# Kernel tuning notes

Measured on AMD Instinct MI355X. Metric: run time of the kernel, lower is better.

## Reference

```python
import jax, jax.numpy as jnp
import numpy as np

K = 10          # number of clusters (static; matches randint fill_max)
ALPHA = 0.02    # intra-cluster margin
DELTA = 0.5     # inter-cluster margin
LAMBDA_INTRA = 1.0
LAMBDA_INTER = 1.0
MIN_WEIGHT = 50.0


def setup_inputs() -> dict:
    key = jax.random.key(0)
    k1, k2 = jax.random.split(key)
    x = jax.random.normal(k1, (8, 64, 240, 320), dtype=jnp.float32)
    # module assumes NORMALIZED unit vectors along channel dim
    x = x / jnp.maximum(jnp.linalg.norm(x, axis=1, keepdims=True), 1e-12)
    cluster_masks = jax.random.randint(k2, (8, 1, 240, 320), 0, K, dtype=jnp.int32)
    return {"x": x, "cluster_masks": cluster_masks}


def reference(x, cluster_masks):
    B, C, H, W = x.shape
    cm = cluster_masks[:, 0]  # (B, H, W) int
    # one-hot cluster assignment; out-of-range ids (e.g. -1 = unlabeled) -> all zeros
    onehot = jax.nn.one_hot(cm, K, dtype=x.dtype)  # (B, H, W, K)

    # ---- spherical cluster means (fused segment-reduce over H*W) ----
    sums = jnp.einsum('bchw,bhwk->bck', x, onehot)          # (B, C, K)
    counts = jnp.sum(onehot, axis=(1, 2))                    # (B, K)
    means = sums / (counts[:, None, :] + 1e-10)
    # F.normalize(p=2, dim=1): x / max(||x||, eps)
    means = means / jnp.maximum(jnp.linalg.norm(means, axis=1, keepdims=True), 1e-12)

    # ---- broadcast means back to pixels ----
    tiled = jnp.einsum('bck,bhwk->bchw', means, onehot)      # (B, C, H, W)

    labeled = (cm >= 0).astype(x.dtype)                      # (B, H, W)
    # cosine metric
    intra_d = labeled * (0.5 * (1.0 - jnp.sum(x * tiled, axis=1)))  # (B, H, W)

    # ---- per-cluster hard-example weighting ----
    indicator = (intra_d > ALPHA).astype(x.dtype)            # (B, H, W)
    N_k = jnp.einsum('bhw,bhwk->bk', indicator, onehot)      # (B, K)
    weights = jnp.einsum('bk,bhwk->bhw', N_k, onehot)        # (B, H, W)
    weights = jnp.maximum(weights, MIN_WEIGHT) * K
    intra_loss = jnp.sum(intra_d ** 2 / weights) / B
    intra_loss = LAMBDA_INTRA * jnp.where(jnp.sum(indicator) > 0, intra_loss, 0.0)

    # ---- inter-cluster hinge loss (K > 1 statically) ----
    inter_d = 0.5 * (1.0 - jnp.einsum('bck,bcl->bkl', means, means))  # (B, K, K)
    hinge = jnp.maximum(DELTA - inter_d, 0.0) * (1.0 - jnp.eye(K, dtype=x.dtype))
    inter_loss = LAMBDA_INTER * jnp.sum(hinge ** 2) / (K * (K - 1) / 2 * B)

    loss = intra_loss + inter_loss
    return (loss, intra_loss, inter_loss)
```

## Files before the change

kernel.cpp:

```cpp
#include <hip/hip_runtime.h>

#define B_ 8
#define C_ 64
#define H_ 240
#define W_ 320
#define HW_ (H_ * W_)
#define HW4_ (HW_ / 4)
#define K_ 10
#define ALPHA_ 0.02f
#define DELTA_ 0.5f
#define MIN_WEIGHT_ 50.0f

#define NCH 4
#define CB_ (C_ / NCH)
#define Z1 8
#define CHUNK1 (HW4_ / Z1)

#define OFF_SUMS 0
#define OFF_CNT  5120
#define OFF_S2   5200
#define OFF_NK   5280
#define OFF_MEANS 5360

__global__ __launch_bounds__(256) void k1_sums(
    const float* __restrict__ x, const int* __restrict__ cm,
    float* __restrict__ ws) {
  const int cb = blockIdx.x;
  const int b = blockIdx.y;
  const int z = blockIdx.z;
  const int tid = threadIdx.x;
  const int c0 = cb * NCH;

  const int lo = z * CHUNK1;
  const int hi = lo + CHUNK1;

  float* __restrict__ sums = ws + OFF_SUMS;
  float* __restrict__ counts = ws + OFF_CNT;

  const float4* __restrict__ xp =
      (const float4*)(x + (size_t)(b * C_ + c0) * HW_);
  const int4* __restrict__ cp = (const int4*)(cm + (size_t)b * HW_);

  float acc[NCH][K_];
#pragma unroll
  for (int c = 0; c < NCH; ++c)
#pragma unroll
    for (int j = 0; j < K_; ++j) acc[c][j] = 0.f;
  float cnt[K_];
#pragma unroll
  for (int j = 0; j < K_; ++j) cnt[j] = 0.f;
  const bool do_cnt = (cb == 0);

  for (int i = lo + tid; i < hi; i += 256) {
    const int4 k4 = cp[i];
    float oh0[K_], oh1[K_], oh2[K_], oh3[K_];
#pragma unroll
    for (int j = 0; j < K_; ++j) {
      oh0[j] = (k4.x == j) ? 1.f : 0.f;
      oh1[j] = (k4.y == j) ? 1.f : 0.f;
      oh2[j] = (k4.z == j) ? 1.f : 0.f;
      oh3[j] = (k4.w == j) ? 1.f : 0.f;
    }
    if (do_cnt) {
#pragma unroll
      for (int j = 0; j < K_; ++j)
        cnt[j] += (oh0[j] + oh1[j]) + (oh2[j] + oh3[j]);
    }
#pragma unroll
    for (int c = 0; c < NCH; ++c) {
      const float4 v = xp[c * HW4_ + i];
#pragma unroll
      for (int j = 0; j < K_; ++j) {
        acc[c][j] += v.x * oh0[j];
        acc[c][j] += v.y * oh1[j];
        acc[c][j] += v.z * oh2[j];
        acc[c][j] += v.w * oh3[j];
      }
    }
  }

#pragma unroll
  for (int c = 0; c < NCH; ++c) {
#pragma unroll
    for (int j = 0; j < K_; ++j) {
      float v = acc[c][j];
#pragma unroll
      for (int off = 32; off > 0; off >>= 1) v += __shfl_down(v, off, 64);
      if ((tid & 63) == 0)
        atomicAdd(&sums[(b * C_ + c0 + c) * K_ + j], v);
    }
  }
  if (do_cnt) {
#pragma unroll
    for (int j = 0; j < K_; ++j) {
      float v = cnt[j];
#pragma unroll
      for (int off = 32; off > 0; off >>= 1) v += __shfl_down(v, off, 64);
      if ((tid & 63) == 0) atomicAdd(&counts[b * K_ + j], v);
    }
  }
}

__global__ __launch_bounds__(256) void k2_norm(float* __restrict__ ws) {
  const int b = blockIdx.x;
  const int tid = threadIdx.x;

  const float* __restrict__ sums = ws + OFF_SUMS + b * C_ * K_;
  const float* __restrict__ counts = ws + OFF_CNT + b * K_;
  float* __restrict__ means = ws + OFF_MEANS + b * C_ * K_;

  __shared__ float mlds[C_ * K_];
  __shared__ float nrm[K_];

  for (int i = tid; i < C_ * K_; i += 256)
    mlds[i] = sums[i] / (counts[i % K_] + 1e-10f);
  __syncthreads();
  if (tid < K_) {
    float n2 = 0.f;
#pragma unroll
    for (int c = 0; c < C_; ++c) {
      const float mm = mlds[c * K_ + tid];
      n2 += mm * mm;
    }
    nrm[tid] = 1.f / fmaxf(sqrtf(n2), 1e-12f);
  }
  __syncthreads();
  for (int i = tid; i < C_ * K_; i += 256)
    means[i] = mlds[i] * nrm[i % K_];
}

__global__ __launch_bounds__(128) void k3_intra(
    const float* __restrict__ x, const int* __restrict__ cm,
    float* __restrict__ ws) {
  const int b = blockIdx.y;
  const int tid = threadIdx.x;
  const int w = tid >> 6;

  float* __restrict__ S2 = ws + OFF_S2;
  float* __restrict__ Nk = ws + OFF_NK;
  const float* __restrict__ means = ws + OFF_MEANS;

  __shared__ float mlds[C_ * K_];
  __shared__ float s2w[2 * K_];
  __shared__ float nkw[2 * K_];

  for (int i = tid; i < C_ * K_; i += 128) mlds[i] = means[b * C_ * K_ + i];
  if (tid < 2 * K_) { s2w[tid] = 0.f; nkw[tid] = 0.f; }
  __syncthreads();

  const int p4 = blockIdx.x * 128 + tid;
  const int4 k4 = ((const int4*)(cm + (size_t)b * HW_))[p4];
  const float4* __restrict__ xb =
      (const float4*)(x + (size_t)b * C_ * HW_) + p4;

  const float* __restrict__ m0 = &mlds[k4.x];
  const float* __restrict__ m1 = &mlds[k4.y];
  const float* __restrict__ m2 = &mlds[k4.z];
  const float* __restrict__ m3 = &mlds[k4.w];

  float d0 = 0.f, d1 = 0.f, d2 = 0.f, d3 = 0.f;
#pragma unroll 16
  for (int c = 0; c < C_; ++c) {
    const float4 v = xb[c * HW4_];
    d0 += v.x * m0[c * K_];
    d1 += v.y * m1[c * K_];
    d2 += v.z * m2[c * K_];
    d3 += v.w * m3[c * K_];
  }

  const float i0 = 0.5f * (1.f - d0);
  const float i1 = 0.5f * (1.f - d1);
  const float i2 = 0.5f * (1.f - d2);
  const float i3 = 0.5f * (1.f - d3);

  atomicAdd(&s2w[w * K_ + k4.x], i0 * i0);
  atomicAdd(&s2w[w * K_ + k4.y], i1 * i1);
  atomicAdd(&s2w[w * K_ + k4.z], i2 * i2);
  atomicAdd(&s2w[w * K_ + k4.w], i3 * i3);
  atomicAdd(&nkw[w * K_ + k4.x], i0 > ALPHA_ ? 1.f : 0.f);
  atomicAdd(&nkw[w * K_ + k4.y], i1 > ALPHA_ ? 1.f : 0.f);
  atomicAdd(&nkw[w * K_ + k4.z], i2 > ALPHA_ ? 1.f : 0.f);
  atomicAdd(&nkw[w * K_ + k4.w], i3 > ALPHA_ ? 1.f : 0.f);
  __syncthreads();

  if (tid < K_) {
    atomicAdd(&S2[b * K_ + tid], s2w[tid] + s2w[K_ + tid]);
    atomicAdd(&Nk[b * K_ + tid], nkw[tid] + nkw[K_ + tid]);
  }
}

__global__ __launch_bounds__(256) void k4_final(
    const float* __restrict__ ws, float* __restrict__ out) {
  const int tid = threadIdx.x;
  const float* __restrict__ means = ws + OFF_MEANS;
  const float* __restrict__ S2 = ws + OFF_S2;
  const float* __restrict__ Nk = ws + OFF_NK;

  float acc_h = 0.f;
  for (int t = tid; t < B_ * 45; t += 256) {
    const int b = t / 45;
    int idx = t % 45;
    int k = 0, l = 0;
    for (k = 0; k < K_; ++k) {
      const int row = K_ - 1 - k;
      if (idx < row) { l = k + 1 + idx; break; }
      idx -= row;
    }
    float g = 0.f;
    for (int c = 0; c < C_; ++c)
      g += means[(b * C_ + c) * K_ + k] * means[(b * C_ + c) * K_ + l];
    const float inter_d = 0.5f * (1.f - g);
    const float h = fmaxf(DELTA_ - inter_d, 0.f);
    acc_h += 2.f * h * h;
  }

  float acc_i = 0.f, acc_n = 0.f;
  if (tid < B_ * K_) {
    const float nk = Nk[tid];
    acc_n = nk;
    const float w = fmaxf(nk, MIN_WEIGHT_) * (float)K_;
    acc_i = S2[tid] / w;
  }

  __shared__ float rh[256], ri[256], rn[256];
  rh[tid] = acc_h;
  ri[tid] = acc_i;
  rn[tid] = acc_n;
  __syncthreads();
  for (int s = 128; s > 0; s >>= 1) {
    if (tid < s) {
      rh[tid] += rh[tid + s];
      ri[tid] += ri[tid + s];
      rn[tid] += rn[tid + s];
    }
    __syncthreads();
  }
  if (tid == 0) {
    const float inter = rh[0] / (float)((K_ * (K_ - 1) / 2) * B_);
    float intra = ri[0] / (float)B_;
    if (!(rn[0] > 0.f)) intra = 0.f;
    out[0] = intra + inter;
    out[1] = intra;
    out[2] = inter;
  }
}

extern "C" void kernel_launch(void* const* d_in, const int* in_sizes, int n_in,
                              void* d_out, int out_size, void* d_ws, size_t ws_size,
                              hipStream_t stream) {
  const float* x = (const float*)d_in[0];
  const int* cm = (const int*)d_in[1];
  float* ws = (float*)d_ws;

  hipMemsetAsync(d_ws, 0, 5360 * sizeof(float), stream);

  k1_sums<<<dim3(CB_, B_, Z1), 256, 0, stream>>>(x, cm, ws);
  k2_norm<<<B_, 256, 0, stream>>>(ws);
  k3_intra<<<dim3(HW4_ / 128, B_), 128, 0, stream>>>(x, cm, ws);
  k4_final<<<1, 256, 0, stream>>>(ws, (float*)d_out);
}
```

Before: 283.4 us.

## Replace global atomics with per-slice partials and drop workspace memset

k1 now reduces each block's wave results through shared memory and writes them to a per-z-slice partial buffer instead of issuing global atomicAdds. k2 sums the slices, zeroes the S2/Nk accumulators itself, and computes the per-batch inter-cluster hinge in parallel across 45 threads. That lets k4 shrink to a simple reduction and removes the hipMemsetAsync launch. The intent is to remove atomic contention, one memset launch and the serial work in k4, at the cost of a larger workspace and extra reads in k2.

```diff
diff --git a/kernel.cpp b/kernel.cpp
--- a/kernel.cpp
+++ b/kernel.cpp
@@ -16,11 +16,12 @@
 #define Z1 8
 #define CHUNK1 (HW4_ / Z1)
 
-#define OFF_SUMS 0
-#define OFF_CNT  5120
-#define OFF_S2   5200
-#define OFF_NK   5280
-#define OFF_MEANS 5360
+#define SL_SUMS 0
+#define SL_CNT  (Z1 * B_ * C_ * K_)
+#define OFF_S2  (SL_CNT + Z1 * B_ * K_)
+#define OFF_NK  (OFF_S2 + B_ * K_)
+#define OFF_HP  (OFF_NK + B_ * K_)
+#define OFF_MEANS 41792
 
 __global__ __launch_bounds__(256) void k1_sums(
     const float* __restrict__ x, const int* __restrict__ cm,
@@ -34,9 +35,6 @@
   const int lo = z * CHUNK1;
   const int hi = lo + CHUNK1;
 
-  float* __restrict__ sums = ws + OFF_SUMS;
-  float* __restrict__ counts = ws + OFF_CNT;
-
   const float4* __restrict__ xp =
       (const float4*)(x + (size_t)(b * C_ + c0) * HW_);
   const int4* __restrict__ cp = (const int4*)(cm + (size_t)b * HW_);
@@ -79,6 +77,9 @@
     }
   }
 
+  __shared__ float partS[4][NCH * K_];
+  __shared__ float partC[4][K_];
+  const int w = tid >> 6;
 #pragma unroll
   for (int c = 0; c < NCH; ++c) {
 #pragma unroll
@@ -86,8 +87,7 @@
       float v = acc[c][j];
 #pragma unroll
       for (int off = 32; off > 0; off >>= 1) v += __shfl_down(v, off, 64);
-      if ((tid & 63) == 0)
-        atomicAdd(&sums[(b * C_ + c0 + c) * K_ + j], v);
+      if ((tid & 63) == 0) partS[w][c * K_ + j] = v;
     }
   }
   if (do_cnt) {
@@ -96,8 +96,18 @@
       float v = cnt[j];
 #pragma unroll
       for (int off = 32; off > 0; off >>= 1) v += __shfl_down(v, off, 64);
-      if ((tid & 63) == 0) atomicAdd(&counts[b * K_ + j], v);
-    }
+      if ((tid & 63) == 0) partC[w][j] = v;
+    }
+  }
+  __syncthreads();
+
+  float* __restrict__ slice =
+      ws + SL_SUMS + z * (B_ * C_ * K_) + (b * C_ + c0) * K_;
+  if (tid < NCH * K_)
+    slice[tid] = (partS[0][tid] + partS[1][tid]) + (partS[2][tid] + partS[3][tid]);
+  if (do_cnt && tid < K_) {
+    ws[SL_CNT + z * (B_ * K_) + b * K_ + tid] =
+        (partC[0][tid] + partC[1][tid]) + (partC[2][tid] + partC[3][tid]);
   }
 }
 
@@ -105,15 +115,29 @@
   const int b = blockIdx.x;
   const int tid = threadIdx.x;
 
-  const float* __restrict__ sums = ws + OFF_SUMS + b * C_ * K_;
-  const float* __restrict__ counts = ws + OFF_CNT + b * K_;
   float* __restrict__ means = ws + OFF_MEANS + b * C_ * K_;
 
   __shared__ float mlds[C_ * K_];
+  __shared__ float cntl[K_];
   __shared__ float nrm[K_];
-
-  for (int i = tid; i < C_ * K_; i += 256)
-    mlds[i] = sums[i] / (counts[i % K_] + 1e-10f);
+  __shared__ float hr[64];
+
+  if (tid < K_) {
+    float s = 0.f;
+#pragma unroll
+    for (int z = 0; z < Z1; ++z) s += ws[SL_CNT + z * (B_ * K_) + b * K_ + tid];
+    cntl[tid] = s;
+    ws[OFF_S2 + b * K_ + tid] = 0.f;
+    ws[OFF_NK + b * K_ + tid] = 0.f;
+  }
+  __syncthreads();
+  for (int i = tid; i < C_ * K_; i += 256) {
+    float s = 0.f;
+#pragma unroll
+    for (int z = 0; z < Z1; ++z)
+      s += ws[SL_SUMS + z * (B_ * C_ * K_) + b * C_ * K_ + i];
+    mlds[i] = s / (cntl[i % K_] + 1e-10f);
+  }
   __syncthreads();
   if (tid < K_) {
     float n2 = 0.f;
@@ -125,8 +149,34 @@
     nrm[tid] = 1.f / fmaxf(sqrtf(n2), 1e-12f);
   }
   __syncthreads();
-  for (int i = tid; i < C_ * K_; i += 256)
-    means[i] = mlds[i] * nrm[i % K_];
+  for (int i = tid; i < C_ * K_; i += 256) {
+    const float m = mlds[i] * nrm[i % K_];
+    mlds[i] = m;
+    means[i] = m;
+  }
+  __syncthreads();
+
+  if (tid < 45) {
+    int idx = tid;
+    int k = 0, l = 0;
+    for (k = 0; k < K_; ++k) {
+      const int row = K_ - 1 - k;
+      if (idx < row) { l = k + 1 + idx; break; }
+      idx -= row;
+    }
+    float g = 0.f;
+#pragma unroll
+    for (int c = 0; c < C_; ++c) g += mlds[c * K_ + k] * mlds[c * K_ + l];
+    const float inter_d = 0.5f * (1.f - g);
+    const float h = fmaxf(DELTA_ - inter_d, 0.f);
+    hr[tid] = 2.f * h * h;
+  }
+  __syncthreads();
+  if (tid == 0) {
+    float s = 0.f;
+    for (int i = 0; i < 45; ++i) s += hr[i];
+    ws[OFF_HP + b] = s;
+  }
 }
 
 __global__ __launch_bounds__(128) void k3_intra(
@@ -189,45 +239,28 @@
   }
 }
 
-__global__ __launch_bounds__(256) void k4_final(
+__global__ __launch_bounds__(128) void k4_final(
     const float* __restrict__ ws, float* __restrict__ out) {
   const int tid = threadIdx.x;
-  const float* __restrict__ means = ws + OFF_MEANS;
   const float* __restrict__ S2 = ws + OFF_S2;
   const float* __restrict__ Nk = ws + OFF_NK;
-
-  float acc_h = 0.f;
-  for (int t = tid; t < B_ * 45; t += 256) {
-    const int b = t / 45;
-    int idx = t % 45;
-    int k = 0, l = 0;
-    for (k = 0; k < K_; ++k) {
-      const int row = K_ - 1 - k;
-      if (idx < row) { l = k + 1 + idx; break; }
-      idx -= row;
-    }
-    float g = 0.f;
-    for (int c = 0; c < C_; ++c)
-      g += means[(b * C_ + c) * K_ + k] * means[(b * C_ + c) * K_ + l];
-    const float inter_d = 0.5f * (1.f - g);
-    const float h = fmaxf(DELTA_ - inter_d, 0.f);
-    acc_h += 2.f * h * h;
-  }
-
-  float acc_i = 0.f, acc_n = 0.f;
+  const float* __restrict__ hp = ws + OFF_HP;
+
+  float acc_i = 0.f, acc_n = 0.f, acc_h = 0.f;
   if (tid < B_ * K_) {
     const float nk = Nk[tid];
     acc_n = nk;
     const float w = fmaxf(nk, MIN_WEIGHT_) * (float)K_;
     acc_i = S2[tid] / w;
   }
-
-  __shared__ float rh[256], ri[256], rn[256];
+  if (tid < B_) acc_h = hp[tid];
+
+  __shared__ float rh[128], ri[128], rn[128];
   rh[tid] = acc_h;
   ri[tid] = acc_i;
   rn[tid] = acc_n;
   __syncthreads();
-  for (int s = 128; s > 0; s >>= 1) {
+  for (int s = 64; s > 0; s >>= 1) {
     if (tid < s) {
       rh[tid] += rh[tid + s];
       ri[tid] += ri[tid + s];
@@ -252,10 +285,8 @@
   const int* cm = (const int*)d_in[1];
   float* ws = (float*)d_ws;
 
-  hipMemsetAsync(d_ws, 0, 5360 * sizeof(float), stream);
-
   k1_sums<<<dim3(CB_, B_, Z1), 256, 0, stream>>>(x, cm, ws);
   k2_norm<<<B_, 256, 0, stream>>>(ws);
   k3_intra<<<dim3(HW4_ / 128, B_), 128, 0, stream>>>(x, cm, ws);
-  k4_final<<<1, 256, 0, stream>>>(ws, (float*)d_out);
-}
+  k4_final<<<1, 128, 0, stream>>>(ws, (float*)d_out);
+}
```

New measurement: 271.9 us. -4.1%, faster.
